# Performance work log

Hardware: AMD Instinct MI355X
Metric: run time of the kernel (lower is better)

The kernel has to match this reference:

```python
import jax, jax.numpy as jnp
import numpy as np

D_MODEL = 1024
N_HEADS = 16
HEAD_DIM = D_MODEL // N_HEADS


def setup_inputs() -> dict:
    key = jax.random.key(0)
    ks = jax.random.split(key, 9)
    B, T = 2, 2048
    s = 1.0 / np.sqrt(D_MODEL)
    x = jax.random.normal(ks[0], (B, T, D_MODEL), dtype=jnp.float32)
    Wq = jax.random.uniform(ks[1], (D_MODEL, D_MODEL), jnp.float32, -s, s)
    bq = jax.random.uniform(ks[2], (D_MODEL,), jnp.float32, -s, s)
    Wk = jax.random.uniform(ks[3], (D_MODEL, D_MODEL), jnp.float32, -s, s)
    bk = jax.random.uniform(ks[4], (D_MODEL,), jnp.float32, -s, s)
    Wv = jax.random.uniform(ks[5], (D_MODEL, D_MODEL), jnp.float32, -s, s)
    bv = jax.random.uniform(ks[6], (D_MODEL,), jnp.float32, -s, s)
    Wp = jax.random.uniform(ks[7], (D_MODEL, D_MODEL), jnp.float32, -s, s)
    bp = jax.random.uniform(ks[8], (D_MODEL,), jnp.float32, -s, s)
    return {"x": x, "Wq": Wq, "bq": bq, "Wk": Wk, "bk": bk,
            "Wv": Wv, "bv": bv, "Wp": Wp, "bp": bp}


def reference(x, Wq, bq, Wk, bk, Wv, bv, Wp, bp):
    B, T, C = x.shape
    H, Dh = N_HEADS, HEAD_DIM
    # torch Linear: x @ W.T + b
    q = (x @ Wq.T + bq).reshape(B, T, H, Dh).transpose(0, 2, 1, 3)  # [B,H,T,Dh]
    k = (x @ Wk.T + bk).reshape(B, T, H, Dh).transpose(0, 2, 1, 3)
    v = (x @ Wv.T + bv).reshape(B, T, H, Dh).transpose(0, 2, 1, 3)
    scale = 1.0 / np.sqrt(Dh).astype(np.float32)
    att = jnp.einsum('bhqd,bhkd->bhqk', q, k) * scale  # [B,H,T,T]
    causal = jnp.tril(jnp.ones((T, T), dtype=bool))
    att = jnp.where(causal[None, None], att, -jnp.inf)
    att = jax.nn.softmax(att, axis=-1)
    y = jnp.einsum('bhqk,bhkd->bhqd', att, v)  # [B,H,T,Dh]
    y = y.transpose(0, 2, 1, 3).reshape(B, T, C)
    return y @ Wp.T + bp
```

## Files before the change

kernel.cpp:

```cpp
#include <hip/hip_runtime.h>
#include <math.h>

#define D_MODEL 1024
#define N_HEADS 16
#define HEAD_DIM 64
#define SEQ_T 2048
#define BATCH 2

typedef __attribute__((ext_vector_type(8))) short short8;
typedef __attribute__((ext_vector_type(4))) float f32x4;

__device__ __forceinline__ unsigned short f2bf(float f) {
    union { float f; unsigned int u; } v; v.f = f;
    return (unsigned short)((v.u + 0x7FFFu + ((v.u >> 16) & 1u)) >> 16);
}

__device__ __forceinline__ unsigned short f2bf_fast(float f) {
    union { float f; unsigned int u; } v; v.f = f;
    return (unsigned short)((v.u + 0x8000u) >> 16);
}

__device__ __forceinline__ void glds16(const unsigned short* g, unsigned short* l) {
    __builtin_amdgcn_global_load_lds(
        (const __attribute__((address_space(1))) unsigned int*)g,
        (__attribute__((address_space(3))) unsigned int*)l, 16, 0, 0);
}

__global__ void cvt_all(const float4* __restrict__ x,
                        const float4* __restrict__ Wq, const float4* __restrict__ Wk,
                        const float4* __restrict__ Wv, const float4* __restrict__ Wp,
                        ushort4* __restrict__ xb, ushort4* __restrict__ wb,
                        ushort4* __restrict__ wpb) {
    int i = blockIdx.x * 256 + threadIdx.x;
    float4 v; ushort4* dst;
    if (i < 1048576) { v = x[i]; dst = xb + i; }
    else {
        int j = i - 1048576;
        int wsel = j >> 18;
        int o = j & 262143;
        const float4* s = wsel == 0 ? Wq : wsel == 1 ? Wk : wsel == 2 ? Wv : Wp;
        v = s[o];
        dst = (wsel == 3) ? (wpb + o) : (wb + (size_t)wsel * 262144 + o);
    }
    ushort4 u;
    u.x = f2bf(v.x); u.y = f2bf(v.y); u.z = f2bf(v.z); u.w = f2bf(v.w);
    *dst = u;
}

template<int MODE, int MTILE>
__global__ __launch_bounds__(256) void gemm2(
    const unsigned short* __restrict__ A,
    const unsigned short* __restrict__ W,
    const float* __restrict__ b0, const float* __restrict__ b1, const float* __restrict__ b2,
    void* __restrict__ o0, void* __restrict__ o1, void* __restrict__ o2)
{
    constexpr int K = 1024;
    constexpr int MT = MTILE / 32;
    constexpr int CAW = MTILE / 64;
    __shared__ unsigned short As[MTILE * 32];
    __shared__ unsigned short Bs[128 * 32];
    const int m0 = blockIdx.y * MTILE;
    const int n0 = blockIdx.x * 128;
    const int tid = threadIdx.x;
    const int w = tid >> 6, lane = tid & 63;
    const int col = lane & 15, quad = lane >> 4;
    const int wm = (w & 1) * (MTILE / 2), wn = (w >> 1) * 64;
    const int lr = lane >> 2, lc = (lane & 3) * 8;

    const f32x4 zero = {0.f, 0.f, 0.f, 0.f};
    f32x4 acc[MT][4];
#pragma unroll
    for (int i = 0; i < MT; i++)
#pragma unroll
        for (int j = 0; j < 4; j++) acc[i][j] = zero;

    for (int k0 = 0; k0 < K; k0 += 32) {
        __syncthreads();
#pragma unroll
        for (int c = 0; c < CAW; c++) {
            const int q = w * CAW + c;
            glds16(&A[(size_t)(m0 + q * 16 + lr) * K + k0 + lc], &As[q * 512]);
        }
#pragma unroll
        for (int c = 0; c < 2; c++) {
            const int q = w * 2 + c;
            glds16(&W[(size_t)(n0 + q * 16 + lr) * K + k0 + lc], &Bs[q * 512]);
        }
        __syncthreads();
        short8 af[MT], bf[4];
#pragma unroll
        for (int mt = 0; mt < MT; mt++)
            af[mt] = *(const short8*)&As[(wm + mt * 16 + col) * 32 + quad * 8];
#pragma unroll
        for (int nt = 0; nt < 4; nt++)
            bf[nt] = *(const short8*)&Bs[(wn + nt * 16 + col) * 32 + quad * 8];
#pragma unroll
        for (int mt = 0; mt < MT; mt++)
#pragma unroll
            for (int nt = 0; nt < 4; nt++)
                acc[mt][nt] = __builtin_amdgcn_mfma_f32_16x16x32_bf16(af[mt], bf[nt], acc[mt][nt], 0, 0, 0);
    }

#pragma unroll
    for (int mt = 0; mt < MT; mt++) {
#pragma unroll
        for (int nt = 0; nt < 4; nt++) {
            const int n = n0 + wn + nt * 16 + col;
            float bias;
            if constexpr (MODE == 2) bias = b0[n];
            else {
                const int sel = n >> 10, nq = n & 1023;
                bias = (sel == 0 ? b0 : sel == 1 ? b1 : b2)[nq];
            }
#pragma unroll
            for (int r = 0; r < 4; r++) {
                const int m = m0 + wm + mt * 16 + quad * 4 + r;
                const float v = acc[mt][nt][r] + bias;
                if constexpr (MODE == 2) {
                    ((float*)o0)[(size_t)m * 1024 + n] = v;
                } else {
                    const int sel = n >> 10, nq = n & 1023;
                    const int h = nq >> 6, dh = nq & 63, b = m >> 11, t = m & 2047;
                    if (sel < 2) {
                        unsigned short* dst = sel ? (unsigned short*)o1 : (unsigned short*)o0;
                        int tt = t;
                        if (sel == 1) {
                            const int tb = t & 31;
                            tt = (t & ~31) + ((tb & 4) << 2) + ((tb >> 3) << 2) + (tb & 3);
                        }
                        dst[(((size_t)(b * N_HEADS + h)) * SEQ_T + tt) * HEAD_DIM + dh] = f2bf(v);
                    } else {
                        ((unsigned short*)o2)[((size_t)(b * N_HEADS + h) * HEAD_DIM + dh) * SEQ_T + t] = f2bf(v);
                    }
                }
            }
        }
    }
}

__global__ __launch_bounds__(256) void flash7(
    const unsigned short* __restrict__ Q,
    const unsigned short* __restrict__ Kp,
    const unsigned short* __restrict__ Vt,
    unsigned short* __restrict__ Y)
{
    __shared__ unsigned short Ks[2][64 * 64];
    __shared__ unsigned short Vs[2][64 * 64];

    const int tid = threadIdx.x;
    const int w = tid >> 6, lane = tid & 63;
    const int col = lane & 15, quad = lane >> 4;
    const int i = blockIdx.x;
    const int bh = (i & 7) * 4 + ((i >> 3) & 3);
    const int qtp = i >> 5;
    const int b = bh >> 4, h = bh & 15;

    const unsigned short* qbase = Q + (size_t)bh * SEQ_T * HEAD_DIM;
    const unsigned short* kbase = Kp + (size_t)bh * SEQ_T * HEAD_DIM;
    const unsigned short* vbase = Vt + (size_t)bh * HEAD_DIM * SEQ_T;

    const int srow = lane >> 3;
    const int schunk = (lane & 7) ^ srow;
    const int cswz = col & 7;

    const float SC = 0.125f;
    const f32x4 zero = {0.f, 0.f, 0.f, 0.f};

    for (int ti = 0; ti < 2; ti++) {
        const int qt = ti ? (31 - qtp) : qtp;
        const int qrow = qt * 64 + w * 16;
        const short8 qf0 = *(const short8*)&qbase[(size_t)(qrow + col) * HEAD_DIM + quad * 8];
        const short8 qf1 = *(const short8*)&qbase[(size_t)(qrow + col) * HEAD_DIM + quad * 8 + 32];

        f32x4 acc[4];
#pragma unroll
        for (int nt = 0; nt < 4; nt++) acc[nt] = zero;
        float l = 0.f;

        const int nk = qt + 1;

        __syncthreads();
#pragma unroll
        for (int rq = 0; rq < 2; rq++) {
            const int rr = rq * 32 + 8 * w;
            glds16(&kbase[(size_t)(rr + srow) * HEAD_DIM + schunk * 8], &Ks[0][rr * 64]);
            glds16(&vbase[(size_t)(rr + srow) * SEQ_T + schunk * 8], &Vs[0][rr * 64]);
        }

        int cur = 0;
        for (int kt = 0; kt < nk; kt++) {
            const int kb = kt * 64;
            __syncthreads();

            if (kt + 1 < nk) {
                const int kb2 = kb + 64;
#pragma unroll
                for (int rq = 0; rq < 2; rq++) {
                    const int rr = rq * 32 + 8 * w;
                    glds16(&kbase[(size_t)(kb2 + rr + srow) * HEAD_DIM + schunk * 8], &Ks[cur ^ 1][rr * 64]);
                    glds16(&vbase[(size_t)(rr + srow) * SEQ_T + kb2 + schunk * 8], &Vs[cur ^ 1][rr * 64]);
                }
            }

            const unsigned short* ks = Ks[cur];
            const unsigned short* vs = Vs[cur];

            short8 vB[2][4];
#pragma unroll
            for (int g = 0; g < 2; g++)
#pragma unroll
                for (int nt = 0; nt < 4; nt++)
                    vB[g][nt] = *(const short8*)&vs[(nt * 16 + col) * 64 + (((g * 4 + quad) ^ cswz) * 8)];

            f32x4 St[4];
#pragma unroll
            for (int kc = 0; kc < 4; kc++) {
                const short8 kf0 = *(const short8*)&ks[(kc * 16 + col) * 64 + ((quad ^ cswz) * 8)];
                const short8 kf1 = *(const short8*)&ks[(kc * 16 + col) * 64 + (((quad + 4) ^ cswz) * 8)];
                f32x4 z = zero;
                z = __builtin_amdgcn_mfma_f32_16x16x32_bf16(kf0, qf0, z, 0, 0, 0);
                z = __builtin_amdgcn_mfma_f32_16x16x32_bf16(kf1, qf1, z, 0, 0, 0);
                St[kc] = z;
            }

            const bool diag = (kt == nk - 1);
            short8 pA[2];
#pragma unroll
            for (int g = 0; g < 2; g++) {
#pragma unroll
                for (int t16 = 0; t16 < 2; t16++) {
                    const int kc = 2 * g + t16;
                    const int kbase_c = kb + (kc >> 1) * 32 + quad * 8 + (kc & 1) * 4;
#pragma unroll
                    for (int r = 0; r < 4; r++) {
                        float p = __expf(St[kc][r] * SC);
                        if (diag && (kbase_c + r > qrow + col)) p = 0.f;
                        l += p;
                        pA[g][t16 * 4 + r] = (short)f2bf_fast(p);
                    }
                }
            }

#pragma unroll
            for (int g = 0; g < 2; g++)
#pragma unroll
                for (int nt = 0; nt < 4; nt++)
                    acc[nt] = __builtin_amdgcn_mfma_f32_16x16x32_bf16(pA[g], vB[g][nt], acc[nt], 0, 0, 0);

            cur ^= 1;
        }

        l += __shfl_xor(l, 16);
        l += __shfl_xor(l, 32);
        const float linv = 1.0f / l;
        float lr[4];
#pragma unroll
        for (int r = 0; r < 4; r++) lr[r] = __shfl(linv, quad * 4 + r);
#pragma unroll
        for (int nt = 0; nt < 4; nt++)
#pragma unroll
            for (int r = 0; r < 4; r++) {
                const int qg = qrow + quad * 4 + r;
                Y[((size_t)(b * SEQ_T + qg)) * D_MODEL + h * HEAD_DIM + nt * 16 + col] = f2bf(acc[nt][r] * lr[r]);
            }
    }
}

extern "C" void kernel_launch(void* const* d_in, const int* in_sizes, int n_in,
                              void* d_out, int out_size, void* d_ws, size_t ws_size,
                              hipStream_t stream) {
    const float* x  = (const float*)d_in[0];
    const float* Wq = (const float*)d_in[1];
    const float* bq = (const float*)d_in[2];
    const float* Wk = (const float*)d_in[3];
    const float* bk = (const float*)d_in[4];
    const float* Wv = (const float*)d_in[5];
    const float* bv = (const float*)d_in[6];
    const float* Wp = (const float*)d_in[7];
    const float* bp = (const float*)d_in[8];
    float* out = (float*)d_out;

    char* ws = (char*)d_ws;
    const size_t XSZ = (size_t)4096 * 1024 * 2;
    unsigned short* xb  = (unsigned short*)ws;  ws += XSZ;
    unsigned short* wb  = (unsigned short*)ws;  ws += (size_t)3072 * 1024 * 2;
    unsigned short* wpb = (unsigned short*)ws;  ws += (size_t)1024 * 1024 * 2;
    unsigned short* qb  = (unsigned short*)ws;  ws += XSZ;
    unsigned short* kb  = (unsigned short*)ws;  ws += XSZ;
    unsigned short* vtb = (unsigned short*)ws;  ws += XSZ;
    unsigned short* yb  = (unsigned short*)ws;  ws += XSZ;

    cvt_all<<<8192, 256, 0, stream>>>((const float4*)x, (const float4*)Wq, (const float4*)Wk,
                                      (const float4*)Wv, (const float4*)Wp,
                                      (ushort4*)xb, (ushort4*)wb, (ushort4*)wpb);

    gemm2<3, 128><<<dim3(24, 32), 256, 0, stream>>>(xb, wb, bq, bk, bv, qb, kb, vtb);

    flash7<<<512, 256, 0, stream>>>(qb, kb, vtb, yb);

    gemm2<2, 64><<<dim3(8, 64), 256, 0, stream>>>(yb, wpb, bp, nullptr, nullptr, out, nullptr, nullptr);
}
```

Baseline: 183.3 us.

## Deepen GEMM K-step to 64 with XOR-swizzled LDS and transposed V projection

The GEMM k-loop now stages 64-wide K slices per iteration, halving the barrier count, and uses an XOR swizzle on the LDS chunk index to avoid bank conflicts on fragment reads. The QKV kernel becomes a 1D grid where the V projection blocks compute Wv·xᵀ, so the transposed V output is written with t contiguous instead of strided scattered stores. This doubles LDS use per block and adds block-index branching and a per-element bias lookup for the V path.

```diff
diff --git a/kernel.cpp b/kernel.cpp
--- a/kernel.cpp
+++ b/kernel.cpp
@@ -56,16 +56,30 @@
 {
     constexpr int K = 1024;
     constexpr int MT = MTILE / 32;
-    constexpr int CAW = MTILE / 64;
-    __shared__ unsigned short As[MTILE * 32];
-    __shared__ unsigned short Bs[128 * 32];
-    const int m0 = blockIdx.y * MTILE;
-    const int n0 = blockIdx.x * 128;
+    constexpr int CAW = MTILE / 32;
+    __shared__ unsigned short As[MTILE * 64];
+    __shared__ unsigned short Bs[128 * 64];
     const int tid = threadIdx.x;
     const int w = tid >> 6, lane = tid & 63;
     const int col = lane & 15, quad = lane >> 4;
     const int wm = (w & 1) * (MTILE / 2), wn = (w >> 1) * 64;
-    const int lr = lane >> 2, lc = (lane & 3) * 8;
+    const int srow = lane >> 3;
+    const int schunk = (lane & 7) ^ srow;
+
+    const unsigned short* Aop; const unsigned short* Bop;
+    int m0, n0; bool isV = false;
+    if constexpr (MODE == 3) {
+        const int bid = blockIdx.x;
+        if (bid < 512) { n0 = (bid & 15) << 7; m0 = (bid >> 4) << 7; Aop = A; Bop = W; }
+        else {
+            const int j = bid - 512; isV = true;
+            n0 = (j & 31) << 7; m0 = (j >> 5) << 7;
+            Aop = W + ((size_t)2 << 20);
+            Bop = A;
+        }
+    } else {
+        m0 = blockIdx.y * MTILE; n0 = blockIdx.x * 128; Aop = A; Bop = W;
+    }
 
     const f32x4 zero = {0.f, 0.f, 0.f, 0.f};
     f32x4 acc[MT][4];
@@ -74,31 +88,38 @@
 #pragma unroll
         for (int j = 0; j < 4; j++) acc[i][j] = zero;
 
-    for (int k0 = 0; k0 < K; k0 += 32) {
+    for (int k0 = 0; k0 < K; k0 += 64) {
         __syncthreads();
 #pragma unroll
         for (int c = 0; c < CAW; c++) {
             const int q = w * CAW + c;
-            glds16(&A[(size_t)(m0 + q * 16 + lr) * K + k0 + lc], &As[q * 512]);
-        }
-#pragma unroll
-        for (int c = 0; c < 2; c++) {
-            const int q = w * 2 + c;
-            glds16(&W[(size_t)(n0 + q * 16 + lr) * K + k0 + lc], &Bs[q * 512]);
+            glds16(&Aop[(size_t)(m0 + q * 8 + srow) * K + k0 + schunk * 8], &As[q * 512]);
+        }
+#pragma unroll
+        for (int c = 0; c < 4; c++) {
+            const int q = w * 4 + c;
+            glds16(&Bop[(size_t)(n0 + q * 8 + srow) * K + k0 + schunk * 8], &Bs[q * 512]);
         }
         __syncthreads();
-        short8 af[MT], bf[4];
-#pragma unroll
-        for (int mt = 0; mt < MT; mt++)
-            af[mt] = *(const short8*)&As[(wm + mt * 16 + col) * 32 + quad * 8];
-#pragma unroll
-        for (int nt = 0; nt < 4; nt++)
-            bf[nt] = *(const short8*)&Bs[(wn + nt * 16 + col) * 32 + quad * 8];
-#pragma unroll
-        for (int mt = 0; mt < MT; mt++)
-#pragma unroll
-            for (int nt = 0; nt < 4; nt++)
-                acc[mt][nt] = __builtin_amdgcn_mfma_f32_16x16x32_bf16(af[mt], bf[nt], acc[mt][nt], 0, 0, 0);
+#pragma unroll
+        for (int kk = 0; kk < 2; kk++) {
+            short8 af[MT], bf[4];
+#pragma unroll
+            for (int mt = 0; mt < MT; mt++) {
+                const int r = wm + mt * 16 + col;
+                af[mt] = *(const short8*)&As[r * 64 + ((((kk << 2) | quad) ^ (r & 7)) << 3)];
+            }
+#pragma unroll
+            for (int nt = 0; nt < 4; nt++) {
+                const int r = wn + nt * 16 + col;
+                bf[nt] = *(const short8*)&Bs[r * 64 + ((((kk << 2) | quad) ^ (r & 7)) << 3)];
+            }
+#pragma unroll
+            for (int mt = 0; mt < MT; mt++)
+#pragma unroll
+                for (int nt = 0; nt < 4; nt++)
+                    acc[mt][nt] = __builtin_amdgcn_mfma_f32_16x16x32_bf16(af[mt], bf[nt], acc[mt][nt], 0, 0, 0);
+        }
     }
 
 #pragma unroll
@@ -106,22 +127,19 @@
 #pragma unroll
         for (int nt = 0; nt < 4; nt++) {
             const int n = n0 + wn + nt * 16 + col;
-            float bias;
+            float bias = 0.f;
             if constexpr (MODE == 2) bias = b0[n];
-            else {
-                const int sel = n >> 10, nq = n & 1023;
-                bias = (sel == 0 ? b0 : sel == 1 ? b1 : b2)[nq];
-            }
+            else { if (!isV) bias = (n < 1024 ? b0 : b1)[n & 1023]; }
 #pragma unroll
             for (int r = 0; r < 4; r++) {
                 const int m = m0 + wm + mt * 16 + quad * 4 + r;
-                const float v = acc[mt][nt][r] + bias;
                 if constexpr (MODE == 2) {
-                    ((float*)o0)[(size_t)m * 1024 + n] = v;
+                    ((float*)o0)[(size_t)m * 1024 + n] = acc[mt][nt][r] + bias;
                 } else {
-                    const int sel = n >> 10, nq = n & 1023;
-                    const int h = nq >> 6, dh = nq & 63, b = m >> 11, t = m & 2047;
-                    if (sel < 2) {
+                    if (!isV) {
+                        const int sel = n >> 10, nq = n & 1023;
+                        const int h = nq >> 6, dh = nq & 63, b = m >> 11, t = m & 2047;
+                        const float v = acc[mt][nt][r] + bias;
                         unsigned short* dst = sel ? (unsigned short*)o1 : (unsigned short*)o0;
                         int tt = t;
                         if (sel == 1) {
@@ -130,6 +148,8 @@
                         }
                         dst[(((size_t)(b * N_HEADS + h)) * SEQ_T + tt) * HEAD_DIM + dh] = f2bf(v);
                     } else {
+                        const int h = m >> 6, dh = m & 63, b = n >> 11, t = n & 2047;
+                        const float v = acc[mt][nt][r] + b2[m];
                         ((unsigned short*)o2)[((size_t)(b * N_HEADS + h) * HEAD_DIM + dh) * SEQ_T + t] = f2bf(v);
                     }
                 }
@@ -294,7 +314,7 @@
                                       (const float4*)Wv, (const float4*)Wp,
                                       (ushort4*)xb, (ushort4*)wb, (ushort4*)wpb);
 
-    gemm2<3, 128><<<dim3(24, 32), 256, 0, stream>>>(xb, wb, bq, bk, bv, qb, kb, vtb);
+    gemm2<3, 128><<<768, 256, 0, stream>>>(xb, wb, bq, bk, bv, qb, kb, vtb);
 
     flash7<<<512, 256, 0, stream>>>(qb, kb, vtb, yb);
 
```

Result: slower. 198.8 us (+8.4%).

## Replace QKV projection GEMM with 256x256-tile pipelined gemm8 kernel

Applied to the files above, without the earlier changes.

Adds a new QKV projection kernel that uses 256x256 output tiles with 512 threads and swizzled LDS layouts. A and B tiles are double buffered through direct global-to-LDS loads, staggered across the four compute sub-steps, and MFMA sections run at raised wave priority. The larger tile is meant to raise arithmetic intensity and overlap loads with MFMA compared with the 128x128 gemm2. In exchange it launches only 192 blocks, so CU utilisation is limited, and it uses 128 KB of LDS per block plus heavy register pressure.

```diff
diff --git a/kernel.cpp b/kernel.cpp
--- a/kernel.cpp
+++ b/kernel.cpp
@@ -45,6 +45,146 @@
     ushort4 u;
     u.x = f2bf(v.x); u.y = f2bf(v.y); u.z = f2bf(v.z); u.w = f2bf(v.w);
     *dst = u;
+}
+
+__device__ __forceinline__ void stage_half8(const unsigned short* __restrict__ src,
+                                            int row0, int k0, unsigned short* dst,
+                                            int w, int srow, int schunk) {
+#pragma unroll
+    for (int c = 0; c < 2; c++) {
+        const int rb = (w * 2 + c) * 8;
+        glds16(&src[(size_t)(row0 + rb + srow) * 1024 + k0 + schunk * 8], &dst[rb * 64]);
+    }
+}
+
+__global__ __launch_bounds__(512, 2) void gemm8(
+    const unsigned short* __restrict__ A,
+    const unsigned short* __restrict__ W,
+    const float* __restrict__ b0, const float* __restrict__ b1, const float* __restrict__ b2,
+    unsigned short* __restrict__ o0, unsigned short* __restrict__ o1,
+    unsigned short* __restrict__ o2)
+{
+    __shared__ unsigned short As[2][16384];
+    __shared__ unsigned short Bs[2][16384];
+
+    const int tid = threadIdx.x;
+    const int w = tid >> 6, lane = tid & 63;
+    const int col = lane & 15, quad = lane >> 4;
+    const int wr = w >> 2, wc = w & 3;
+    const int bid = blockIdx.x;
+    const int mi = bid / 12, ni = bid % 12;
+    const int m0 = mi * 256, n0 = ni * 256;
+    const int srow = lane >> 3;
+    const int schunk = (lane & 7) ^ srow;
+    const int cswz = col & 7;
+
+    const f32x4 zero = {0.f, 0.f, 0.f, 0.f};
+    f32x4 acc[8][4];
+#pragma unroll
+    for (int i = 0; i < 8; i++)
+#pragma unroll
+        for (int j = 0; j < 4; j++) acc[i][j] = zero;
+
+    stage_half8(A, m0,        0, As[0],        w, srow, schunk);
+    stage_half8(A, m0 + 128,  0, As[0] + 8192, w, srow, schunk);
+    stage_half8(W, n0,        0, Bs[0],        w, srow, schunk);
+    stage_half8(W, n0 + 128,  0, Bs[0] + 8192, w, srow, schunk);
+    stage_half8(W, n0,       64, Bs[1],        w, srow, schunk);
+    stage_half8(W, n0 + 128, 64, Bs[1] + 8192, w, srow, schunk);
+    asm volatile("s_waitcnt vmcnt(4)" ::: "memory");
+    __builtin_amdgcn_s_barrier();
+
+    for (int tau = 0; tau < 16; tau++) {
+        const int cur = tau & 1;
+        const unsigned short* as = As[cur];
+        const unsigned short* bs = Bs[cur];
+        unsigned short* asN = As[cur ^ 1];
+        unsigned short* bsN = Bs[cur];
+        const int kA = tau * 64 + 64;
+        const int kB = tau * 64 + 128;
+        short8 bf[4][2];
+
+#pragma unroll
+        for (int q = 0; q < 4; q++) {
+            short8 af[2][2];
+#pragma unroll
+            for (int f2 = 0; f2 < 2; f2++) {
+                const int r = wr * 128 + (q * 2 + f2) * 16 + col;
+#pragma unroll
+                for (int kk = 0; kk < 2; kk++)
+                    af[f2][kk] = *(const short8*)&as[r * 64 + ((((kk << 2) | quad) ^ cswz) << 3)];
+            }
+            if (q == 0) {
+#pragma unroll
+                for (int nt = 0; nt < 4; nt++) {
+                    const int r = wc * 64 + nt * 16 + col;
+#pragma unroll
+                    for (int kk = 0; kk < 2; kk++)
+                        bf[nt][kk] = *(const short8*)&bs[r * 64 + ((((kk << 2) | quad) ^ cswz) << 3)];
+                }
+            }
+            if (q == 0 && tau + 1 < 16) stage_half8(A, m0,       kA, asN,        w, srow, schunk);
+            if (q == 1 && tau + 1 < 16) stage_half8(A, m0 + 128, kA, asN + 8192, w, srow, schunk);
+            if (q == 2 && tau + 2 < 16) stage_half8(W, n0,       kB, bsN,        w, srow, schunk);
+            if (q == 3) {
+                if (tau + 2 < 16) {
+                    stage_half8(W, n0 + 128, kB, bsN + 8192, w, srow, schunk);
+                    asm volatile("s_waitcnt vmcnt(4)" ::: "memory");
+                } else if (tau + 1 < 16) {
+                    asm volatile("s_waitcnt vmcnt(0)" ::: "memory");
+                }
+            }
+            if (q == 0) asm volatile("s_waitcnt lgkmcnt(8)" ::: "memory");
+            __builtin_amdgcn_s_barrier();
+            asm volatile("s_waitcnt lgkmcnt(0)" ::: "memory");
+            __builtin_amdgcn_s_setprio(1);
+#pragma unroll
+            for (int kk = 0; kk < 2; kk++)
+#pragma unroll
+                for (int f2 = 0; f2 < 2; f2++)
+#pragma unroll
+                    for (int nt = 0; nt < 4; nt++)
+                        acc[q * 2 + f2][nt] = __builtin_amdgcn_mfma_f32_16x16x32_bf16(
+                            af[f2][kk], bf[nt][kk], acc[q * 2 + f2][nt], 0, 0, 0);
+            __builtin_amdgcn_s_setprio(0);
+            __builtin_amdgcn_s_barrier();
+        }
+    }
+
+    const int sel = n0 >> 10;
+    const float* bsrc = sel == 0 ? b0 : sel == 1 ? b1 : b2;
+#pragma unroll
+    for (int fr = 0; fr < 8; fr++) {
+        const int mbase = m0 + wr * 128 + fr * 16 + quad * 4;
+        const int b = mbase >> 11, t = mbase & 2047;
+#pragma unroll
+        for (int nt = 0; nt < 4; nt++) {
+            const int nq = (n0 & 1023) + wc * 64 + nt * 16 + col;
+            const int h = nq >> 6, dh = nq & 63;
+            const float bias = bsrc[nq];
+            if (sel < 2) {
+                unsigned short* dst = sel ? o1 : o0;
+#pragma unroll
+                for (int r = 0; r < 4; r++) {
+                    const int tr = t + r;
+                    int tt = tr;
+                    if (sel == 1) {
+                        const int tb = tr & 31;
+                        tt = (tr & ~31) + ((tb & 4) << 2) + ((tb >> 3) << 2) + (tb & 3);
+                    }
+                    dst[(((size_t)(b * N_HEADS + h)) * SEQ_T + tt) * HEAD_DIM + dh] =
+                        f2bf(acc[fr][nt][r] + bias);
+                }
+            } else {
+                ushort4 u;
+                u.x = f2bf(acc[fr][nt][0] + bias);
+                u.y = f2bf(acc[fr][nt][1] + bias);
+                u.z = f2bf(acc[fr][nt][2] + bias);
+                u.w = f2bf(acc[fr][nt][3] + bias);
+                *(ushort4*)&o2[((size_t)(b * N_HEADS + h) * HEAD_DIM + dh) * SEQ_T + t] = u;
+            }
+        }
+    }
 }
 
 template<int MODE, int MTILE>
@@ -294,7 +434,7 @@
                                       (const float4*)Wv, (const float4*)Wp,
                                       (ushort4*)xb, (ushort4*)wb, (ushort4*)wpb);
 
-    gemm2<3, 128><<<dim3(24, 32), 256, 0, stream>>>(xb, wb, bq, bk, bv, qb, kb, vtb);
+    gemm8<<<192, 512, 0, stream>>>(xb, wb, bq, bk, bv, qb, kb, vtb);
 
     flash7<<<512, 256, 0, stream>>>(qb, kb, vtb, yb);
 
```

Result: slower. 190.3 us (+3.8%).
